# Performance work log

Measured on AMD Instinct MI355X. Metric: run time of the kernel, lower is better.

The kernel has to match this reference:

```python
import jax, jax.numpy as jnp
import numpy as np

B, S, D, H = 2, 2048, 1024, 16
DH = D // H

def setup_inputs() -> dict:
    key = jax.random.key(0)
    ks = jax.random.split(key, 12)
    inp = {
        'query': jax.random.normal(ks[0], (B, S, D), jnp.float32),
        'key':   jax.random.normal(ks[1], (B, S, D), jnp.float32),
        'value': jax.random.normal(ks[2], (B, S, D), jnp.float32),
        # causal mask: 1.0 where attention is DISALLOWED (added as mask * -1e9)
        'mask': jnp.triu(jnp.ones((S, S), jnp.float32), k=1)[None, None, :, :],
    }
    sc = 1.0 / np.sqrt(D)
    inp['Wq'] = jax.random.normal(ks[3], (D, D), jnp.float32) * sc
    inp['bq'] = jnp.zeros((D,), jnp.float32)
    inp['Wk'] = jax.random.normal(ks[4], (D, D), jnp.float32) * sc
    inp['bk'] = jnp.zeros((D,), jnp.float32)
    inp['Wv'] = jax.random.normal(ks[5], (D, D), jnp.float32) * sc
    inp['bv'] = jnp.zeros((D,), jnp.float32)
    inp['Wo'] = jax.random.normal(ks[6], (D, D), jnp.float32) * sc
    inp['bo'] = jnp.zeros((D,), jnp.float32)
    return inp

def _split_heads(x):
    # [B,S,D] -> [B,H,S,DH]
    b, s, _ = x.shape
    return x.reshape(b, s, H, DH).transpose(0, 2, 1, 3)

def reference(query, key, value, mask, Wq, bq, Wk, bk, Wv, bv, Wo, bo):
    q = _split_heads(query @ Wq + bq)
    k = _split_heads(key @ Wk + bk)
    v = _split_heads(value @ Wv + bv)
    scale = jnp.sqrt(jnp.asarray(DH, jnp.float32))
    # [B,H,S,S] score tensor (naive, unfused — matches original)
    score = jnp.einsum('bhqd,bhkd->bhqk', q, k) / scale
    score = score + mask * (-1e9)
    attn = jax.nn.softmax(score, axis=-1)
    ctx = jnp.einsum('bhqk,bhkd->bhqd', attn, v)
    ctx = ctx.transpose(0, 2, 1, 3).reshape(query.shape[0], -1, D)
    return ctx @ Wo + bo
```

## Files before the change

### kernel.cpp

```cpp
#include <hip/hip_runtime.h>
#include <hip/hip_bf16.h>
#include <stdint.h>


typedef __bf16 bf16;
typedef __bf16 bf16x2v __attribute__((ext_vector_type(2)));
typedef __bf16 bf16x4v __attribute__((ext_vector_type(4)));
typedef __bf16 bf16x8v __attribute__((ext_vector_type(8)));
typedef float  f32x4v  __attribute__((ext_vector_type(4)));
typedef float  f32x16v __attribute__((ext_vector_type(16)));
typedef unsigned int uint32x2v __attribute__((ext_vector_type(2)));

#define MFMA32(a, b, c) __builtin_amdgcn_mfma_f32_32x32x16_bf16((a), (b), (c), 0, 0, 0)
#define MFMA16(a, b, c) __builtin_amdgcn_mfma_f32_16x16x32_bf16((a), (b), (c), 0, 0, 0)
#define LGKM0() asm volatile("s_waitcnt lgkmcnt(0)" ::: "memory")

static constexpr int kS = 2048, kD = 1024, kH = 16, kDH = 64, kM = 4096;

__device__ __forceinline__ void gload16(const void* g, void* lds) {
  __builtin_amdgcn_global_load_lds((const __attribute__((address_space(1))) void*)g,
                                   (__attribute__((address_space(3))) void*)lds, 16, 0, 0);
}

__device__ __forceinline__ float fexp2(float x) {
#if __has_builtin(__builtin_amdgcn_exp2f)
  return __builtin_amdgcn_exp2f(x);
#else
  return exp2f(x);
#endif
}

__global__ void __launch_bounds__(256) cvt_x_kernel(
    const float* __restrict__ q, const float* __restrict__ k, const float* __restrict__ v,
    bf16* __restrict__ xq, bf16* __restrict__ xk, bf16* __restrict__ xv) {
  int i = (blockIdx.x * 256 + threadIdx.x) * 4;
  float4 a = *(const float4*)(q + i);
  float4 b = *(const float4*)(k + i);
  float4 c = *(const float4*)(v + i);
  bf16x4v oa = {(bf16)a.x, (bf16)a.y, (bf16)a.z, (bf16)a.w};
  bf16x4v ob = {(bf16)b.x, (bf16)b.y, (bf16)b.z, (bf16)b.w};
  bf16x4v oc = {(bf16)c.x, (bf16)c.y, (bf16)c.z, (bf16)c.w};
  *(bf16x4v*)(xq + i) = oa;
  *(bf16x4v*)(xk + i) = ob;
  *(bf16x4v*)(xv + i) = oc;
}

__global__ void __launch_bounds__(256) cvt_w_kernel(
    const float* __restrict__ w0, const float* __restrict__ w1,
    const float* __restrict__ w2, const float* __restrict__ w3,
    bf16* __restrict__ o0, bf16* __restrict__ o1, bf16* __restrict__ o2, bf16* __restrict__ o3) {
  const float* w = blockIdx.z == 0 ? w0 : blockIdx.z == 1 ? w1 : blockIdx.z == 2 ? w2 : w3;
  bf16* o       = blockIdx.z == 0 ? o0 : blockIdx.z == 1 ? o1 : blockIdx.z == 2 ? o2 : o3;
  __shared__ float t[32][33];
  int tx = threadIdx.x, ty = threadIdx.y;
  int k0 = blockIdx.x * 32, n0 = blockIdx.y * 32;
#pragma unroll
  for (int j = 0; j < 4; ++j)
    t[ty + j * 8][tx] = w[(size_t)(k0 + ty + j * 8) * kD + n0 + tx];
  __syncthreads();
#pragma unroll
  for (int j = 0; j < 4; ++j)
    o[(size_t)(n0 + ty + j * 8) * kD + k0 + tx] = (bf16)t[tx][ty + j * 8];
}

struct GemmArgs {
  const bf16* A;
  const bf16* Wt;
  const float* bias;
  void* out;
  float scale;
  int omode;
};

__global__ void __launch_bounds__(256) gemm_kernel(GemmArgs ga, GemmArgs gb, GemmArgs gc) {
  GemmArgs g = blockIdx.z == 0 ? ga : blockIdx.z == 1 ? gb : gc;
  constexpr int BN = 64, WN = 32, NJ = 2;
  constexpr int ASZ = 128 * 32;
  constexpr int BSZ = BN * 32;
  __shared__ __align__(16) bf16 smem[2 * ASZ + 2 * BSZ];
  const int tid = threadIdx.x, wid = tid >> 6, lane = tid & 63;
  const int g4 = lane >> 4, l16 = lane & 15;
  const int m0 = blockIdx.x * 128, n0 = blockIdx.y * BN;
  const int wr = wid >> 1, wc = wid & 1;
  const bf16* Wt = g.Wt;

  auto stageA = [&](int k0, bf16* As) {
#pragma unroll
    for (int i = 0; i < 2; ++i) {
      int id = i * 256 + tid;
      int row = id >> 2, c = id & 3;
      gload16(g.A + (size_t)(m0 + row) * kD + k0 + ((c ^ ((row >> 1) & 3)) * 8),
              As + (i * 256 + wid * 64) * 8);
    }
  };
  auto stageB = [&](int k0, bf16* Bs) {
    int row = tid >> 2, c = tid & 3;
    gload16(Wt + (size_t)(n0 + row) * kD + k0 + ((c ^ ((row >> 1) & 3)) * 8),
            Bs + (wid * 64) * 8);
  };

  const int xorv = (l16 >> 1) & 3;
  f32x4v acc[4][NJ] = {};

  stageA(0, smem);
  stageB(0, smem + 2 * ASZ);
  __syncthreads();

  constexpr int NT = kD / 32;
  for (int t = 0; t < NT; ++t) {
    const int c = t & 1;
    bf16* Asc = smem + c * ASZ;
    bf16* Bsc = smem + 2 * ASZ + c * BSZ;
    if (t + 1 < NT) {
      stageA((t + 1) * 32, smem + (c ^ 1) * ASZ);
      stageB((t + 1) * 32, smem + 2 * ASZ + (c ^ 1) * BSZ);
    }
    bf16x8v af[4], bfr[NJ];
#pragma unroll
    for (int i = 0; i < 4; ++i) {
      int rowA = wr * 64 + i * 16 + l16;
      af[i] = *(const bf16x8v*)(Asc + rowA * 32 + ((g4 ^ xorv) * 8));
    }
#pragma unroll
    for (int j = 0; j < NJ; ++j) {
      int rowB = wc * WN + j * 16 + l16;
      bfr[j] = *(const bf16x8v*)(Bsc + rowB * 32 + ((g4 ^ xorv) * 8));
    }
#pragma unroll
    for (int i = 0; i < 4; ++i)
#pragma unroll
      for (int j = 0; j < NJ; ++j)
        acc[i][j] = MFMA16(af[i], bfr[j], acc[i][j]);
    __syncthreads();
  }

  float* bws = (float*)smem + wid * 1152;
  const int bb = m0 >> 11;
  const int h = n0 >> 6;

  if (g.omode == 1) {
    float bj[NJ];
#pragma unroll
    for (int j = 0; j < NJ; ++j) bj[j] = g.bias[n0 + wc * WN + j * 16 + l16];
#pragma unroll
    for (int i = 0; i < 4; ++i) {
#pragma unroll
      for (int j = 0; j < NJ; ++j)
#pragma unroll
        for (int r = 0; r < 4; ++r)
          bws[(g4 * 4 + r) * 36 + j * 16 + l16] = (acc[i][j][r] + bj[j]) * g.scale;
      LGKM0();
#pragma unroll
      for (int cc = 0; cc < 2; ++cc) {
        int id = cc * 64 + lane;
        int row = id >> 3, ch = id & 7;
        f32x4v v = *(const f32x4v*)(bws + row * 36 + ch * 4);
        bf16x4v ov = {(bf16)v.x, (bf16)v.y, (bf16)v.z, (bf16)v.w};
        int srow = (m0 + wr * 64 + i * 16 + row) & (kS - 1);
        *(bf16x4v*)((bf16*)g.out +
                    ((size_t)(bb * kH + h) * kS + srow) * kDH + wc * 32 + ch * 4) = ov;
      }
      LGKM0();
    }
  } else if (g.omode == 2) {
#pragma unroll
    for (int j = 0; j < NJ; ++j) {
      float bj = g.bias[n0 + wc * WN + j * 16 + l16];
#pragma unroll
      for (int i = 0; i < 4; ++i)
#pragma unroll
        for (int r = 0; r < 4; ++r)
          bws[l16 * 72 + i * 16 + g4 * 4 + r] = acc[i][j][r] + bj;
      LGKM0();
#pragma unroll
      for (int cc = 0; cc < 4; ++cc) {
        int id = cc * 64 + lane;
        int row = id >> 4, c = id & 15;
        f32x4v v = *(const f32x4v*)(bws + row * 72 + c * 4);
        bf16x4v ov = {(bf16)v.x, (bf16)v.y, (bf16)v.z, (bf16)v.w};
        int dh = wc * 32 + j * 16 + row;
        int sg = (m0 + wr * 64 + c * 4) & (kS - 1);
        *(bf16x4v*)((bf16*)g.out + ((size_t)(bb * kH + h) * kDH + dh) * kS + sg) = ov;
      }
      LGKM0();
    }
  } else {
    float bj[NJ];
#pragma unroll
    for (int j = 0; j < NJ; ++j) bj[j] = g.bias[n0 + wc * WN + j * 16 + l16];
#pragma unroll
    for (int i = 0; i < 4; ++i) {
#pragma unroll
      for (int j = 0; j < NJ; ++j)
#pragma unroll
        for (int r = 0; r < 4; ++r)
          bws[(g4 * 4 + r) * 36 + j * 16 + l16] = acc[i][j][r] + bj[j];
      LGKM0();
#pragma unroll
      for (int cc = 0; cc < 2; ++cc) {
        int id = cc * 64 + lane;
        int row = id >> 3, ch = id & 7;
        f32x4v v = *(const f32x4v*)(bws + row * 36 + ch * 4);
        int srow = m0 + wr * 64 + i * 16 + row;
        *(f32x4v*)((float*)g.out + (size_t)srow * kD + n0 + wc * 32 + ch * 4) = v;
      }
      LGKM0();
    }
  }
}

__global__ void __launch_bounds__(256) attn_kernel(
    const bf16* __restrict__ Qp, const bf16* __restrict__ Kp,
    const bf16* __restrict__ Vt, bf16* __restrict__ ctx) {
  __shared__ bf16 lds[16384];
  const int tid = threadIdx.x;
  const int wid = tid >> 6, lane = tid & 63;
  const int l32 = lane & 31, hi = lane >> 5;
  const int bh = blockIdx.x;
  const int qt = blockIdx.y;
  const int q0 = qt * 128;
  const int qw = q0 + wid * 32;
  const bf16* Qh = Qp + (size_t)bh * kS * kDH;
  const bf16* Kh = Kp + (size_t)bh * kS * kDH;
  const bf16* Vh = Vt + (size_t)bh * kDH * kS;

  bf16x8v qf[4];
#pragma unroll
  for (int kw = 0; kw < 4; ++kw)
    qf[kw] = *(const bf16x8v*)(Qh + (size_t)(qw + l32) * kDH + kw * 16 + hi * 8);

  f32x16v oacc[2] = {};
  float mreg = -1e30f, lsum = 0.f;
  const int q_lane = qw + l32;

  const int nt = (q0 >> 6) + 2;
  const int ntw = (qw >> 6) + 1;

  const int srow = lane >> 3, schk = lane & 7;
  auto stage = [&](int buf, int k0) {
    bf16* kd = &lds[buf * 8192];
    bf16* vd = kd + 4096;
#pragma unroll
    for (int i = 0; i < 2; ++i) {
      int r = wid * 16 + i * 8 + srow;
      int c = schk ^ (r & 7);
      gload16(Kh + (size_t)(k0 + r) * kDH + c * 8, kd + (wid * 2 + i) * 512);
      gload16(Vh + (size_t)r * kS + k0 + c * 8, vd + (wid * 2 + i) * 512);
    }
  };

  stage(0, 0);
  __syncthreads();
  int cur = 0;
  for (int t = 0; t < nt; ++t) {
    const int k0 = t * 64;
    if (t + 1 < nt) stage(cur ^ 1, k0 + 64);
    if (t < ntw) {
      const bf16* kb = &lds[cur * 8192];
      const bf16* vb = kb + 4096;
      f32x16v st[2] = {};
#pragma unroll
      for (int sub = 0; sub < 2; ++sub) {
        int row = sub * 32 + l32;
        const bf16* krow = kb + row * 64;
        int rx = row & 7;
#pragma unroll
        for (int kw = 0; kw < 4; ++kw) {
          int cw = kw * 2 + hi;
          bf16x8v af = *(const bf16x8v*)(krow + ((cw ^ rx) * 8));
          st[sub] = MFMA32(af, qf[kw], st[sub]);
        }
      }
      if (k0 + 63 > qw) {
#pragma unroll
        for (int sub = 0; sub < 2; ++sub)
#pragma unroll
          for (int r = 0; r < 16; ++r) {
            int kv = k0 + sub * 32 + (r & 3) + 8 * (r >> 2) + 4 * hi;
            if (kv > q_lane) st[sub][r] = -1e30f;
          }
      }
      float rm = st[0][0];
#pragma unroll
      for (int sub = 0; sub < 2; ++sub)
#pragma unroll
        for (int r = 0; r < 16; ++r) rm = fmaxf(rm, st[sub][r]);
      {
        uint32x2v sw = __builtin_amdgcn_permlane32_swap(
            __float_as_uint(rm), __float_as_uint(rm), false, false);
        float partner = __uint_as_float(hi ? sw.x : sw.y);
        rm = fmaxf(rm, partner);
      }
      float mn = fmaxf(mreg, rm);
      float al = fexp2(mreg - mn);
      mreg = mn;
      float rs = 0.f;
#pragma unroll
      for (int sub = 0; sub < 2; ++sub)
#pragma unroll
        for (int r = 0; r < 16; ++r) {
          st[sub][r] = fexp2(st[sub][r] - mn);
          rs += st[sub][r];
        }
      {
        uint32x2v sw = __builtin_amdgcn_permlane32_swap(
            __float_as_uint(rs), __float_as_uint(rs), false, false);
        rs += __uint_as_float(hi ? sw.x : sw.y);
      }
      lsum = lsum * al + rs;
#pragma unroll
      for (int s = 0; s < 2; ++s)
#pragma unroll
        for (int r = 0; r < 16; ++r) oacc[s][r] *= al;

      unsigned int w[16];
#pragma unroll
      for (int sub = 0; sub < 2; ++sub)
#pragma unroll
        for (int i = 0; i < 8; ++i) {
          union { bf16x2v h; unsigned int u; } cv;
          cv.h = bf16x2v{(bf16)st[sub][2 * i], (bf16)st[sub][2 * i + 1]};
          w[sub * 8 + i] = cv.u;
        }
      bf16x8v pb[4];
#pragma unroll
      for (int f = 0; f < 4; ++f) {
        uint32x2v r0 = __builtin_amdgcn_permlane32_swap(w[4 * f], w[4 * f + 2], false, false);
        uint32x2v r1 = __builtin_amdgcn_permlane32_swap(w[4 * f + 1], w[4 * f + 3], false, false);
        union { unsigned int u[4]; bf16x8v h; } fu;
        fu.u[0] = r0.x; fu.u[1] = r1.x; fu.u[2] = r0.y; fu.u[3] = r1.y;
        pb[f] = fu.h;
      }
#pragma unroll
      for (int f = 0; f < 4; ++f) {
        int cw = f * 2 + hi;
#pragma unroll
        for (int s = 0; s < 2; ++s) {
          int row = s * 32 + l32;
          bf16x8v vf = *(const bf16x8v*)(vb + row * 64 + ((cw ^ (row & 7)) * 8));
          oacc[s] = MFMA32(vf, pb[f], oacc[s]);
        }
      }
    }
    __syncthreads();
    cur ^= 1;
  }
  float inv = 1.0f / lsum;
  const int b = bh >> 4, h = bh & 15;
  bf16* crow = ctx + (size_t)(b * kS + qw + l32) * kD + h * 64;
#pragma unroll
  for (int s = 0; s < 2; ++s)
#pragma unroll
    for (int rq = 0; rq < 4; ++rq) {
      union { bf16x4v h; uint32x2v u; } pk;
      pk.h = bf16x4v{(bf16)(oacc[s][rq * 4 + 0] * inv), (bf16)(oacc[s][rq * 4 + 1] * inv),
                     (bf16)(oacc[s][rq * 4 + 2] * inv), (bf16)(oacc[s][rq * 4 + 3] * inv)};
      *(uint32x2v*)(crow + 8 * rq + 4 * hi + 32 * s) = pk.u;
    }
}

extern "C" void kernel_launch(void* const* d_in, const int* in_sizes, int n_in,
                              void* d_out, int out_size, void* d_ws, size_t ws_size,
                              hipStream_t stream) {
  (void)in_sizes; (void)n_in; (void)out_size; (void)ws_size;
  const float* q  = (const float*)d_in[0];
  const float* k  = (const float*)d_in[1];
  const float* v  = (const float*)d_in[2];
  const float* Wq = (const float*)d_in[4];
  const float* bq = (const float*)d_in[5];
  const float* Wk = (const float*)d_in[6];
  const float* bk = (const float*)d_in[7];
  const float* Wv = (const float*)d_in[8];
  const float* bv = (const float*)d_in[9];
  const float* Wo = (const float*)d_in[10];
  const float* bo = (const float*)d_in[11];

  char* p = (char*)d_ws;
  auto carve = [&](size_t bytes) {
    char* r = p;
    p += (bytes + 255) & ~(size_t)255;
    return r;
  };
  const size_t XB = (size_t)kM * kD * sizeof(bf16);
  const size_t WB = (size_t)kD * kD * sizeof(bf16);
  bf16* Xq  = (bf16*)carve(XB);
  bf16* Xk  = (bf16*)carve(XB);
  bf16* Xv  = (bf16*)carve(XB);
  bf16* Wtq = (bf16*)carve(WB);
  bf16* Wtk = (bf16*)carve(WB);
  bf16* Wtv = (bf16*)carve(WB);
  bf16* Wto = (bf16*)carve(WB);
  bf16* Qp  = (bf16*)carve(XB);
  bf16* Kp  = (bf16*)carve(XB);
  bf16* Vt  = (bf16*)carve(XB);
  bf16* Ctx = (bf16*)carve(XB);

  cvt_x_kernel<<<dim3(kM * kD / 1024), 256, 0, stream>>>(q, k, v, Xq, Xk, Xv);
  cvt_w_kernel<<<dim3(32, 32, 4), dim3(32, 8, 1), 0, stream>>>(Wq, Wk, Wv, Wo,
                                                               Wtq, Wtk, Wtv, Wto);
  GemmArgs aq{Xq, Wtq, bq, Qp, 0.125f * 1.44269504f, 1};
  GemmArgs ak{Xk, Wtk, bk, Kp, 1.0f, 1};
  GemmArgs av{Xv, Wtv, bv, Vt, 1.0f, 2};
  gemm_kernel<<<dim3(32, 16, 3), 256, 0, stream>>>(aq, ak, av);
  attn_kernel<<<dim3(32, 16), 256, 0, stream>>>(Qp, Kp, Vt, Ctx);
  GemmArgs ao{Ctx, Wto, bo, d_out, 1.0f, 0};
  gemm_kernel<<<dim3(32, 16, 1), 256, 0, stream>>>(ao, ao, ao);
}
```

Baseline: 239.7 us.

## Retile output GEMM, reorder causal attention blocks, skip redundant softmax rescaling

```diff
diff --git a/kernel.cpp b/kernel.cpp
--- a/kernel.cpp
+++ b/kernel.cpp
@@ -72,21 +72,23 @@
   int omode;
 };
 
+template <int BM>
 __global__ void __launch_bounds__(256) gemm_kernel(GemmArgs ga, GemmArgs gb, GemmArgs gc) {
   GemmArgs g = blockIdx.z == 0 ? ga : blockIdx.z == 1 ? gb : gc;
   constexpr int BN = 64, WN = 32, NJ = 2;
-  constexpr int ASZ = 128 * 32;
+  constexpr int WM = BM / 2, MI = WM / 16;
+  constexpr int ASZ = BM * 32;
   constexpr int BSZ = BN * 32;
   __shared__ __align__(16) bf16 smem[2 * ASZ + 2 * BSZ];
   const int tid = threadIdx.x, wid = tid >> 6, lane = tid & 63;
   const int g4 = lane >> 4, l16 = lane & 15;
-  const int m0 = blockIdx.x * 128, n0 = blockIdx.y * BN;
+  const int m0 = blockIdx.x * BM, n0 = blockIdx.y * BN;
   const int wr = wid >> 1, wc = wid & 1;
   const bf16* Wt = g.Wt;
 
   auto stageA = [&](int k0, bf16* As) {
 #pragma unroll
-    for (int i = 0; i < 2; ++i) {
+    for (int i = 0; i < BM / 64; ++i) {
       int id = i * 256 + tid;
       int row = id >> 2, c = id & 3;
       gload16(g.A + (size_t)(m0 + row) * kD + k0 + ((c ^ ((row >> 1) & 3)) * 8),
@@ -100,7 +102,7 @@
   };
 
   const int xorv = (l16 >> 1) & 3;
-  f32x4v acc[4][NJ] = {};
+  f32x4v acc[MI][NJ] = {};
 
   stageA(0, smem);
   stageB(0, smem + 2 * ASZ);
@@ -115,10 +117,10 @@
       stageA((t + 1) * 32, smem + (c ^ 1) * ASZ);
       stageB((t + 1) * 32, smem + 2 * ASZ + (c ^ 1) * BSZ);
     }
-    bf16x8v af[4], bfr[NJ];
-#pragma unroll
-    for (int i = 0; i < 4; ++i) {
-      int rowA = wr * 64 + i * 16 + l16;
+    bf16x8v af[MI], bfr[NJ];
+#pragma unroll
+    for (int i = 0; i < MI; ++i) {
+      int rowA = wr * WM + i * 16 + l16;
       af[i] = *(const bf16x8v*)(Asc + rowA * 32 + ((g4 ^ xorv) * 8));
     }
 #pragma unroll
@@ -127,7 +129,7 @@
       bfr[j] = *(const bf16x8v*)(Bsc + rowB * 32 + ((g4 ^ xorv) * 8));
     }
 #pragma unroll
-    for (int i = 0; i < 4; ++i)
+    for (int i = 0; i < MI; ++i)
 #pragma unroll
       for (int j = 0; j < NJ; ++j)
         acc[i][j] = MFMA16(af[i], bfr[j], acc[i][j]);
@@ -143,7 +145,7 @@
 #pragma unroll
     for (int j = 0; j < NJ; ++j) bj[j] = g.bias[n0 + wc * WN + j * 16 + l16];
 #pragma unroll
-    for (int i = 0; i < 4; ++i) {
+    for (int i = 0; i < MI; ++i) {
 #pragma unroll
       for (int j = 0; j < NJ; ++j)
 #pragma unroll
@@ -156,7 +158,7 @@
         int row = id >> 3, ch = id & 7;
         f32x4v v = *(const f32x4v*)(bws + row * 36 + ch * 4);
         bf16x4v ov = {(bf16)v.x, (bf16)v.y, (bf16)v.z, (bf16)v.w};
-        int srow = (m0 + wr * 64 + i * 16 + row) & (kS - 1);
+        int srow = (m0 + wr * WM + i * 16 + row) & (kS - 1);
         *(bf16x4v*)((bf16*)g.out +
                     ((size_t)(bb * kH + h) * kS + srow) * kDH + wc * 32 + ch * 4) = ov;
       }
@@ -167,7 +169,7 @@
     for (int j = 0; j < NJ; ++j) {
       float bj = g.bias[n0 + wc * WN + j * 16 + l16];
 #pragma unroll
-      for (int i = 0; i < 4; ++i)
+      for (int i = 0; i < MI; ++i)
 #pragma unroll
         for (int r = 0; r < 4; ++r)
           bws[l16 * 72 + i * 16 + g4 * 4 + r] = acc[i][j][r] + bj;
@@ -179,7 +181,7 @@
         f32x4v v = *(const f32x4v*)(bws + row * 72 + c * 4);
         bf16x4v ov = {(bf16)v.x, (bf16)v.y, (bf16)v.z, (bf16)v.w};
         int dh = wc * 32 + j * 16 + row;
-        int sg = (m0 + wr * 64 + c * 4) & (kS - 1);
+        int sg = (m0 + wr * WM + c * 4) & (kS - 1);
         *(bf16x4v*)((bf16*)g.out + ((size_t)(bb * kH + h) * kDH + dh) * kS + sg) = ov;
       }
       LGKM0();
@@ -189,7 +191,7 @@
 #pragma unroll
     for (int j = 0; j < NJ; ++j) bj[j] = g.bias[n0 + wc * WN + j * 16 + l16];
 #pragma unroll
-    for (int i = 0; i < 4; ++i) {
+    for (int i = 0; i < MI; ++i) {
 #pragma unroll
       for (int j = 0; j < NJ; ++j)
 #pragma unroll
@@ -201,7 +203,7 @@
         int id = cc * 64 + lane;
         int row = id >> 3, ch = id & 7;
         f32x4v v = *(const f32x4v*)(bws + row * 36 + ch * 4);
-        int srow = m0 + wr * 64 + i * 16 + row;
+        int srow = m0 + wr * WM + i * 16 + row;
         *(f32x4v*)((float*)g.out + (size_t)srow * kD + n0 + wc * 32 + ch * 4) = v;
       }
       LGKM0();
@@ -216,8 +218,10 @@
   const int tid = threadIdx.x;
   const int wid = tid >> 6, lane = tid & 63;
   const int l32 = lane & 31, hi = lane >> 5;
-  const int bh = blockIdx.x;
-  const int qt = blockIdx.y;
+  const int bid = blockIdx.x;
+  int qt, bh;
+  if (bid < 256) { qt = bid >> 5; bh = bid & 31; }
+  else           { qt = 15 - ((bid - 256) >> 5); bh = (bid - 256) & 31; }
   const int q0 = qt * 128;
   const int qw = q0 + wid * 32;
   const bf16* Qh = Qp + (size_t)bh * kS * kDH;
@@ -291,15 +295,22 @@
         float partner = __uint_as_float(hi ? sw.x : sw.y);
         rm = fmaxf(rm, partner);
       }
-      float mn = fmaxf(mreg, rm);
-      float al = fexp2(mreg - mn);
-      mreg = mn;
+      if (!__all(rm <= mreg)) {
+        float mn = fmaxf(mreg, rm);
+        float al = fexp2(mreg - mn);
+        mreg = mn;
+        lsum *= al;
+#pragma unroll
+        for (int s = 0; s < 2; ++s)
+#pragma unroll
+          for (int r = 0; r < 16; ++r) oacc[s][r] *= al;
+      }
       float rs = 0.f;
 #pragma unroll
       for (int sub = 0; sub < 2; ++sub)
 #pragma unroll
         for (int r = 0; r < 16; ++r) {
-          st[sub][r] = fexp2(st[sub][r] - mn);
+          st[sub][r] = fexp2(st[sub][r] - mreg);
           rs += st[sub][r];
         }
       {
@@ -307,11 +318,7 @@
             __float_as_uint(rs), __float_as_uint(rs), false, false);
         rs += __uint_as_float(hi ? sw.x : sw.y);
       }
-      lsum = lsum * al + rs;
-#pragma unroll
-      for (int s = 0; s < 2; ++s)
-#pragma unroll
-        for (int r = 0; r < 16; ++r) oacc[s][r] *= al;
+      lsum += rs;
 
       unsigned int w[16];
 #pragma unroll
@@ -401,8 +408,8 @@
   GemmArgs aq{Xq, Wtq, bq, Qp, 0.125f * 1.44269504f, 1};
   GemmArgs ak{Xk, Wtk, bk, Kp, 1.0f, 1};
   GemmArgs av{Xv, Wtv, bv, Vt, 1.0f, 2};
-  gemm_kernel<<<dim3(32, 16, 3), 256, 0, stream>>>(aq, ak, av);
-  attn_kernel<<<dim3(32, 16), 256, 0, stream>>>(Qp, Kp, Vt, Ctx);
+  gemm_kernel<128><<<dim3(32, 16, 3), 256, 0, stream>>>(aq, ak, av);
+  attn_kernel<<<dim3(512), 256, 0, stream>>>(Qp, Kp, Vt, Ctx);
   GemmArgs ao{Ctx, Wto, bo, d_out, 1.0f, 0};
-  gemm_kernel<<<dim3(32, 16, 1), 256, 0, stream>>>(ao, ao, ao);
-}
+  gemm_kernel<64><<<dim3(64, 16, 1), 256, 0, stream>>>(ao, ao, ao);
+}
```

Result: no change. 236.2 us (-1.5%).
